# Performance work log

Measured on AMD Instinct MI355X. Metric: run time of the kernel, lower is better.

The kernel has to match this reference:

```python
import jax, jax.numpy as jnp
import numpy as np

B, S, D, H = 4, 8192, 1024, 16
DH = D // H  # attention head size


def setup_inputs() -> dict:
    key = jax.random.key(0)
    ks = jax.random.split(key, 12)
    sc = 0.02
    return {
        "hidden_states": jax.random.normal(ks[0], (B, S, D), jnp.float32),
        "attention_mask": jnp.zeros((B, 1, S), jnp.float32),
        "Wq": jax.random.normal(ks[1], (D, D), jnp.float32) * sc,
        "bq": jnp.zeros((D,), jnp.float32),
        "Wqa": jax.random.normal(ks[2], (D, H), jnp.float32) * sc,
        "bqa": jnp.zeros((H,), jnp.float32),
        "Wk": jax.random.normal(ks[3], (D, D), jnp.float32) * sc,
        "bk": jnp.zeros((D,), jnp.float32),
        "Wka": jax.random.normal(ks[4], (D, H), jnp.float32) * sc,
        "bka": jnp.zeros((H,), jnp.float32),
        "Wt": jax.random.normal(ks[5], (D, D), jnp.float32) * sc,
        "bt": jnp.zeros((D,), jnp.float32),
    }


def reference(hidden_states, attention_mask, Wq, bq, Wqa, bqa, Wk, bk, Wka, bka, Wt, bt):
    b, s, _ = hidden_states.shape
    scale = 1.0 / np.sqrt(DH).astype(np.float32)

    mixed_q = hidden_states @ Wq + bq            # [B,S,D]
    mixed_k = hidden_states @ Wk + bk            # [B,S,D]

    # query attention pooling: scores [B,H,S]
    q_score = (mixed_q @ Wqa + bqa).transpose(0, 2, 1) * scale + attention_mask
    q_weight = jax.nn.softmax(q_score, axis=-1)  # [B,H,S]

    q_heads = mixed_q.reshape(b, s, H, DH)       # [B,S,H,DH]
    pooled_q = jnp.einsum("bhs,bshd->bhd", q_weight, q_heads)  # [B,H,DH]
    pooled_q = pooled_q.reshape(b, 1, D)         # global query vector per batch

    mixed_qk = mixed_k * pooled_q                # [B,S,D]

    qk_score = (mixed_qk @ Wka + bka).transpose(0, 2, 1) * scale + attention_mask
    qk_weight = jax.nn.softmax(qk_score, axis=-1)  # [B,H,S]

    k_heads = mixed_qk.reshape(b, s, H, DH)
    pooled_k = jnp.einsum("bhs,bshd->bhd", qk_weight, k_heads)  # [B,H,DH]

    weighted = (q_heads * pooled_k[:, None, :, :]).reshape(b, s, D)  # [B,S,D]
    return weighted @ Wt + bt + mixed_q
```

## Files before the change

kernel.cpp:

```cpp
#include <hip/hip_runtime.h>
#include <hip/hip_bf16.h>
#include <stdint.h>

typedef __hip_bfloat16 bf16;
typedef __attribute__((ext_vector_type(8))) short bf16x8v;
typedef __attribute__((ext_vector_type(4))) float f32x4v;

#define B_   4
#define S_   8192
#define D_   1024
#define H_   16
#define DH_  64
#define M_TOT (B_ * S_)

__device__ __forceinline__ float bf2f(bf16 x) { return __bfloat162float(x); }
__device__ __forceinline__ bf16  f2bf(float x) { return __float2bfloat16(x); }

__device__ __forceinline__ void storev(float* p, float v) { *p = v; }
__device__ __forceinline__ void storev(bf16* p, float v) { *p = f2bf(v); }

__device__ __forceinline__ void async_copy16(const void* g, void* l) {
  __builtin_amdgcn_global_load_lds(
      (const __attribute__((address_space(1))) unsigned int*)g,
      (__attribute__((address_space(3))) unsigned int*)l,
      16, 0, 0);
}

#define VMCNT(n) asm volatile("s_waitcnt vmcnt(" #n ")" ::: "memory")
__device__ __forceinline__ void barrier_() {
  asm volatile("" ::: "memory");
  __builtin_amdgcn_s_barrier();
  asm volatile("" ::: "memory");
}

__global__ __launch_bounds__(256) void f2bf_kernel(
    const float* __restrict__ in, bf16* __restrict__ out, int n4)
{
  const int i = blockIdx.x * 256 + threadIdx.x;
  if (i >= n4) return;
  const float4 v = ((const float4*)in)[i];
  union { bf16 h[4]; uint64_t u; } pk;
  pk.h[0] = f2bf(v.x); pk.h[1] = f2bf(v.y);
  pk.h[2] = f2bf(v.z); pk.h[3] = f2bf(v.w);
  ((uint64_t*)out)[i] = pk.u;
}

#define STAGE_A(nb, h, k0) do { \
  async_copy16(gA + (size_t)((h) * 64      ) * sA + (size_t)(k0) * 2, smem + (nb) + (h) * 16384 + ldsw); \
  async_copy16(gA + (size_t)((h) * 64 + 128) * sA + (size_t)(k0) * 2, smem + (nb) + (h) * 16384 + 8192 + ldsw); \
} while (0)

#define STAGE_B(nb, h, k0) do { \
  async_copy16(gB + (size_t)((h) * 32      ) * sB + (size_t)(k0) * 2, smem + (nb) + 32768 + (h) * 16384 + ldsw); \
  async_copy16(gB + (size_t)((h) * 32 + 128) * sB + (size_t)(k0) * 2, smem + (nb) + 32768 + (h) * 16384 + 8192 + ldsw); \
} while (0)

#define READ_A(mh) do { \
  _Pragma("unroll") for (int il = 0; il < 4; ++il) { \
    const uint8_t* p_ = Ab + (mh) * 16384 + (wr * 64 + il * 16 + l16) * 128; \
    a[il][0] = *(const bf16x8v*)(p_ + k0off); \
    a[il][1] = *(const bf16x8v*)(p_ + k1off); } \
} while (0)

#define READ_B(nh, BR) do { \
  _Pragma("unroll") for (int jl = 0; jl < 2; ++jl) { \
    const uint8_t* p_ = Bb + 32768 + (nh) * 16384 + (wc * 32 + jl * 16 + l16) * 128; \
    BR[jl][0] = *(const bf16x8v*)(p_ + k0off); \
    BR[jl][1] = *(const bf16x8v*)(p_ + k1off); } \
} while (0)

#define MFMA_Q(IOFF, JOFF, BR) do { \
  _Pragma("unroll") for (int il = 0; il < 4; ++il) \
  _Pragma("unroll") for (int jl = 0; jl < 2; ++jl) \
  _Pragma("unroll") for (int kk = 0; kk < 2; ++kk) \
    acc[(IOFF) + il][(JOFF) + jl] = __builtin_amdgcn_mfma_f32_16x16x32_bf16( \
        a[il][kk], BR[jl][kk], acc[(IOFF) + il][(JOFF) + jl], 0, 0, 0); \
} while (0)

template <typename OutT>
__global__ __launch_bounds__(512, 2) void gemm256_kernel(
    const bf16* __restrict__ A, int lda, const bf16* __restrict__ BT,
    const float* __restrict__ bias0, const float* __restrict__ bias1,
    const bf16* addC, int ldadd,
    OutT* __restrict__ C, int ldc, int M, int Ncols, int K, int perBatchB)
{
  extern __shared__ __align__(16) uint8_t smem[];

  const int ntile = Ncols >> 8;
  const int mtiles = M >> 8;
  const int xcd = blockIdx.x & 7;
  const int local = blockIdx.x >> 3;
  const int tn = local % ntile;
  const int tm = xcd * (mtiles >> 3) + local / ntile;
  const int m0 = tm << 8, n0 = tn << 8;
  const bf16* Bt = BT + (perBatchB ? (size_t)(m0 >> 13) * (size_t)Ncols * (size_t)K : 0);

  const int tid = threadIdx.x, w = tid >> 6, lane = tid & 63;
  const int quad = lane >> 4, l16 = lane & 15;
  const int wr = w >> 2, wc = w & 3;
  const int lr = lane >> 3, ls = lane & 7;

  const size_t sA = (size_t)lda * 2, sB = (size_t)K * 2;
  const int srcslot = (ls ^ lr) << 4;
  const uint8_t* gA = (const uint8_t*)A  + (size_t)(m0 + 8 * w + lr) * sA + srcslot;
  const uint8_t* gB = (const uint8_t*)Bt + (size_t)(n0 + 64 * wr + 8 * wc + lr) * sB + srcslot;
  const int ldsw = w << 10;

  const int e7 = l16 & 7;
  const int k0off = (quad ^ e7) << 4;
  const int k1off = ((quad + 4) ^ e7) << 4;

  f32x4v acc[8][4] = {};
  bf16x8v a[4][2], b0[2][2], b1[2][2];

  const int NT = K >> 6;

  STAGE_A(0, 0, 0);
  STAGE_B(0, 0, 0);
  STAGE_B(0, 1, 0);
  STAGE_A(0, 1, 0);
  VMCNT(4);
  barrier_();

  for (int t = 0; t < NT; ++t) {
    const int buf = (t & 1) << 16;
    const int nbuf = buf ^ 65536;
    const int kst = (t + 1 < NT ? t + 1 : t) << 6;
    const uint8_t* Ab = smem + buf;
    const uint8_t* Bb = smem + buf;

    READ_A(0);
    READ_B(0, b0);
    STAGE_A(nbuf, 0, kst);
    barrier_();
    __builtin_amdgcn_s_setprio(1);
    MFMA_Q(0, 0, b0);
    __builtin_amdgcn_s_setprio(0);
    VMCNT(4);
    barrier_();

    READ_B(1, b1);
    STAGE_B(nbuf, 0, kst);
    barrier_();
    __builtin_amdgcn_s_setprio(1);
    MFMA_Q(0, 2, b1);
    __builtin_amdgcn_s_setprio(0);
    VMCNT(4);
    barrier_();

    READ_A(1);
    STAGE_B(nbuf, 1, kst);
    barrier_();
    __builtin_amdgcn_s_setprio(1);
    MFMA_Q(4, 2, b1);
    __builtin_amdgcn_s_setprio(0);
    barrier_();

    STAGE_A(nbuf, 1, kst);
    barrier_();
    __builtin_amdgcn_s_setprio(1);
    MFMA_Q(4, 0, b0);
    __builtin_amdgcn_s_setprio(0);
    VMCNT(4);
    barrier_();
  }
  VMCNT(0);

#pragma unroll
  for (int ai = 0; ai < 8; ++ai) {
    const int row = m0 + wr * 128 + ai * 16 + quad * 4;
#pragma unroll
    for (int jb = 0; jb < 4; ++jb) {
      const int col = n0 + wc * 64 + jb * 16 + l16;
      const float bb = (col < 1024) ? (bias0 ? bias0[col] : 0.f)
                                    : (bias1 ? bias1[col - 1024] : 0.f);
      f32x4v v = acc[ai][jb];
#pragma unroll
      for (int r = 0; r < 4; ++r) {
        float o = v[r] + bb;
        if (addC) o += bf2f(addC[(size_t)(row + r) * ldadd + col]);
        storev(&C[(size_t)(row + r) * ldc + col], o);
      }
    }
  }
}

__global__ __launch_bounds__(256) void score_kernel(
    const bf16* __restrict__ X, int ldx, const bf16* __restrict__ WaT,
    float* __restrict__ scores, int perBatchW)
{
  const int tid = threadIdx.x, wave = tid >> 6, lane = tid & 63;
  const int quad = lane >> 4, l16 = lane & 15;
  const int row0 = blockIdx.x * 64 + wave * 16;
  const int b = row0 / S_;
  const bf16* W = WaT + (perBatchW ? (size_t)b * H_ * D_ : 0);
  const bf16* arow = X + (size_t)(row0 + l16) * ldx;
  const bf16* brow = W + (size_t)l16 * D_;
  f32x4v acc = {};
  for (int k0 = 0; k0 < D_; k0 += 32) {
    bf16x8v av = *(const bf16x8v*)(arow + k0 + quad * 8);
    bf16x8v bv = *(const bf16x8v*)(brow + k0 + quad * 8);
    acc = __builtin_amdgcn_mfma_f32_16x16x32_bf16(av, bv, acc, 0, 0, 0);
  }
  const int srel = (row0 % S_) + quad * 4;
  float* orow = scores + ((size_t)b * H_ + l16) * S_ + srel;
#pragma unroll
  for (int r = 0; r < 4; r++) orow[r] = acc[r];
}

__global__ __launch_bounds__(256) void stats_kernel(
    const float* __restrict__ sc, const float* __restrict__ mask,
    float scale, float* __restrict__ stats)
{
  const int bh = blockIdx.x, b = bh >> 4, tid = threadIdx.x;
  const float* row = sc + (size_t)bh * S_;
  const float* mrow = mask + (size_t)b * S_;
  __shared__ float red[256];
  float m = -3.4e38f;
  for (int s = tid; s < S_; s += 256) m = fmaxf(m, row[s] * scale + mrow[s]);
  red[tid] = m; __syncthreads();
  for (int o = 128; o > 0; o >>= 1) { if (tid < o) red[tid] = fmaxf(red[tid], red[tid + o]); __syncthreads(); }
  const float M = red[0]; __syncthreads();
  float sum = 0.f;
  for (int s = tid; s < S_; s += 256) sum += expf(row[s] * scale + mrow[s] - M);
  red[tid] = sum; __syncthreads();
  for (int o = 128; o > 0; o >>= 1) { if (tid < o) red[tid] += red[tid + o]; __syncthreads(); }
  if (tid == 0) { stats[bh * 2] = M; stats[bh * 2 + 1] = red[0]; }
}

__global__ __launch_bounds__(256) void pool_kernel(
    const float* __restrict__ sc, const float* __restrict__ mask,
    const float* __restrict__ stats, const bf16* __restrict__ X, int ldx,
    float* __restrict__ pooled, float scale)
{
  const int bh = blockIdx.x, chunk = blockIdx.y;
  const int b = bh >> 4, h = bh & 15;
  const int dh = threadIdx.x & 63, sr = threadIdx.x >> 6;
  const float M = stats[bh * 2], inv = 1.f / stats[bh * 2 + 1];
  const float* row = sc + (size_t)bh * S_;
  const float* mrow = mask + (size_t)b * S_;
  float acc = 0.f;
  const int s0 = chunk * 256;
  for (int s = s0 + sr; s < s0 + 256; s += 4) {
    float w = expf(row[s] * scale + mrow[s] - M) * inv;
    acc += w * bf2f(X[((size_t)b * S_ + s) * ldx + h * DH_ + dh]);
  }
  __shared__ float red[256];
  red[threadIdx.x] = acc; __syncthreads();
  if (sr == 0)
    atomicAdd(&pooled[b * D_ + h * DH_ + dh],
              red[dh] + red[64 + dh] + red[128 + dh] + red[192 + dh]);
}

__global__ __launch_bounds__(256) void prep_wa_kernel(
    const float* __restrict__ Wa, const float* __restrict__ pq,
    bf16* __restrict__ out, int nb)
{
  const int idx = blockIdx.x * 256 + threadIdx.x;
  if (idx >= nb * H_ * D_) return;
  const int d = idx & (D_ - 1);
  const int h = (idx >> 10) & 15;
  const int b = idx >> 14;
  float v = Wa[d * H_ + h];
  if (pq) v *= pq[b * D_ + d];
  out[idx] = f2bf(v);
}

__global__ __launch_bounds__(1024) void transpose_kernel(
    const float* __restrict__ W, bf16* __restrict__ WT)
{
  __shared__ float t[32][33];
  const int tx = threadIdx.x, ty = threadIdx.y;
  const int bx = blockIdx.x, by = blockIdx.y;
  t[ty][tx] = W[(size_t)(by * 32 + ty) * D_ + bx * 32 + tx];
  __syncthreads();
  WT[(size_t)(bx * 32 + ty) * D_ + by * 32 + tx] = f2bf(t[tx][ty]);
}

__global__ __launch_bounds__(1024) void transpose_scale_kernel(
    const float* __restrict__ W, const float* __restrict__ pq,
    const float* __restrict__ pk, bf16* __restrict__ out)
{
  __shared__ float t[32][33];
  const int tx = threadIdx.x, ty = threadIdx.y;
  const int bx = blockIdx.x, by = blockIdx.y, b = blockIdx.z;
  t[ty][tx] = W[(size_t)(by * 32 + ty) * D_ + bx * 32 + tx];
  __syncthreads();
  const int n = bx * 32 + ty, k = by * 32 + tx;
  const float s = pq[b * D_ + k] * pk[b * D_ + k];
  out[(size_t)b * D_ * D_ + (size_t)n * D_ + k] = f2bf(t[tx][ty] * s);
}

namespace {
struct LdsAttrInit {
  LdsAttrInit() {
    (void)hipFuncSetAttribute(reinterpret_cast<const void*>(&gemm256_kernel<bf16>),
                              hipFuncAttributeMaxDynamicSharedMemorySize, 131072);
    (void)hipFuncSetAttribute(reinterpret_cast<const void*>(&gemm256_kernel<float>),
                              hipFuncAttributeMaxDynamicSharedMemorySize, 131072);
  }
};
LdsAttrInit ldsAttrInit_;
}

extern "C" void kernel_launch(void* const* d_in, const int* in_sizes, int n_in,
                              void* d_out, int out_size, void* d_ws, size_t ws_size,
                              hipStream_t stream)
{
  const float* hs   = (const float*)d_in[0];
  const float* mask = (const float*)d_in[1];
  const float* Wq   = (const float*)d_in[2];
  const float* bq   = (const float*)d_in[3];
  const float* Wqa  = (const float*)d_in[4];
  const float* Wk   = (const float*)d_in[6];
  const float* bk   = (const float*)d_in[7];
  const float* Wka  = (const float*)d_in[8];
  const float* Wt   = (const float*)d_in[10];
  const float* bt   = (const float*)d_in[11];
  float* out = (float*)d_out;

  uint8_t* w = (uint8_t*)d_ws;
  bf16*  hs_bf     = (bf16*)(w + 0);
  bf16*  mixed_qk  = (bf16*)(w + 67108864);
  bf16*  WqkT      = (bf16*)(w + 201326592);
  bf16*  WtTs      = (bf16*)(w + 205520896);
  bf16*  WaqT      = (bf16*)(w + 213909504);
  bf16*  WakTs     = (bf16*)(w + 213942272);
  float* scores_q  = (float*)(w + 214073344);
  float* scores_qk = (float*)(w + 216170496);
  float* stats_q   = (float*)(w + 218267648);
  float* stats_qk  = (float*)(w + 218268160);
  float* pq_raw    = (float*)(w + 218268672);
  float* pk_raw    = (float*)(w + 218285056);

  const bf16* mixed_q = mixed_qk;
  const bf16* mixed_k = mixed_qk + 1024;
  const int LDQK = 2048;

  const float scale = 0.125f;
  dim3 tblk(32, 32);

  f2bf_kernel<<<(M_TOT * D_ / 4 + 255) / 256, 256, 0, stream>>>(hs, hs_bf, M_TOT * D_ / 4);

  transpose_kernel<<<dim3(32, 32), tblk, 0, stream>>>(Wq, WqkT);
  transpose_kernel<<<dim3(32, 32), tblk, 0, stream>>>(Wk, WqkT + 1024 * 1024);

  gemm256_kernel<bf16><<<1024, 512, 131072, stream>>>(
      hs_bf, 1024, WqkT, bq, bk, nullptr, 0, mixed_qk, LDQK, M_TOT, 2048, D_, 0);

  hipMemsetAsync(pq_raw, 0, 2 * D_ * B_ * sizeof(float), stream);

  prep_wa_kernel<<<64, 256, 0, stream>>>(Wqa, nullptr, WaqT, 1);
  score_kernel<<<512, 256, 0, stream>>>(mixed_q, LDQK, WaqT, scores_q, 0);
  stats_kernel<<<64, 256, 0, stream>>>(scores_q, mask, scale, stats_q);
  pool_kernel<<<dim3(64, 32), 256, 0, stream>>>(scores_q, mask, stats_q, mixed_q, LDQK, pq_raw, scale);

  prep_wa_kernel<<<256, 256, 0, stream>>>(Wka, pq_raw, WakTs, 4);
  score_kernel<<<512, 256, 0, stream>>>(mixed_k, LDQK, WakTs, scores_qk, 1);
  stats_kernel<<<64, 256, 0, stream>>>(scores_qk, mask, scale, stats_qk);
  pool_kernel<<<dim3(64, 32), 256, 0, stream>>>(scores_qk, mask, stats_qk, mixed_k, LDQK, pk_raw, scale);

  transpose_scale_kernel<<<dim3(32, 32, 4), tblk, 0, stream>>>(Wt, pq_raw, pk_raw, WtTs);

  gemm256_kernel<float><<<512, 512, 131072, stream>>>(
      mixed_q, LDQK, WtTs, bt, nullptr, mixed_q, LDQK, out, D_, M_TOT, D_, D_, 1);
}
```

Baseline: 626.3 us.

## Unroll GEMM main loop by two, merge transposes, online softmax stats

```diff
diff --git a/kernel.cpp b/kernel.cpp
--- a/kernel.cpp
+++ b/kernel.cpp
@@ -27,6 +27,7 @@
 }
 
 #define VMCNT(n) asm volatile("s_waitcnt vmcnt(" #n ")" ::: "memory")
+#define LGKMCNT(n) asm volatile("s_waitcnt lgkmcnt(" #n ")" ::: "memory")
 __device__ __forceinline__ void barrier_() {
   asm volatile("" ::: "memory");
   __builtin_amdgcn_s_barrier();
@@ -36,13 +37,13 @@
 __global__ __launch_bounds__(256) void f2bf_kernel(
     const float* __restrict__ in, bf16* __restrict__ out, int n4)
 {
-  const int i = blockIdx.x * 256 + threadIdx.x;
-  if (i >= n4) return;
-  const float4 v = ((const float4*)in)[i];
-  union { bf16 h[4]; uint64_t u; } pk;
-  pk.h[0] = f2bf(v.x); pk.h[1] = f2bf(v.y);
-  pk.h[2] = f2bf(v.z); pk.h[3] = f2bf(v.w);
-  ((uint64_t*)out)[i] = pk.u;
+  for (int i = blockIdx.x * 256 + threadIdx.x; i < n4; i += 2048 * 256) {
+    const float4 v = ((const float4*)in)[i];
+    union { bf16 h[4]; uint64_t u; } pk;
+    pk.h[0] = f2bf(v.x); pk.h[1] = f2bf(v.y);
+    pk.h[2] = f2bf(v.z); pk.h[3] = f2bf(v.w);
+    ((uint64_t*)out)[i] = pk.u;
+  }
 }
 
 #define STAGE_A(nb, h, k0) do { \
@@ -75,6 +76,33 @@
   _Pragma("unroll") for (int kk = 0; kk < 2; ++kk) \
     acc[(IOFF) + il][(JOFF) + jl] = __builtin_amdgcn_mfma_f32_16x16x32_bf16( \
         a[il][kk], BR[jl][kk], acc[(IOFF) + il][(JOFF) + jl], 0, 0, 0); \
+} while (0)
+
+#define TILE(BUF, NBUF, KST, DOSTG, W0, W1, W3) do { \
+  const uint8_t* Ab = smem + (BUF); \
+  const uint8_t* Bb = smem + (BUF); \
+   \
+  READ_A(0); READ_B(0, b0); \
+  if (DOSTG) { STAGE_A((NBUF), 0, (KST)); STAGE_B((NBUF), 0, (KST)); } \
+  LGKMCNT(8); \
+  barrier_(); \
+  __builtin_amdgcn_s_setprio(1); MFMA_Q(0, 0, b0); __builtin_amdgcn_s_setprio(0); \
+  W0; barrier_(); \
+   \
+  READ_B(1, b1); \
+  if (DOSTG) { STAGE_B((NBUF), 1, (KST)); } \
+  barrier_(); \
+  __builtin_amdgcn_s_setprio(1); MFMA_Q(0, 2, b1); __builtin_amdgcn_s_setprio(0); \
+  W1; barrier_(); \
+   \
+  READ_A(1); \
+  if (DOSTG) { STAGE_A((NBUF), 1, (KST)); } \
+  barrier_(); \
+  __builtin_amdgcn_s_setprio(1); MFMA_Q(4, 2, b1); __builtin_amdgcn_s_setprio(0); \
+  barrier_(); \
+   \
+  __builtin_amdgcn_s_setprio(1); MFMA_Q(4, 0, b0); __builtin_amdgcn_s_setprio(0); \
+  W3; barrier_(); \
 } while (0)
 
 template <typename OutT>
@@ -122,49 +150,12 @@
   VMCNT(4);
   barrier_();
 
-  for (int t = 0; t < NT; ++t) {
-    const int buf = (t & 1) << 16;
-    const int nbuf = buf ^ 65536;
-    const int kst = (t + 1 < NT ? t + 1 : t) << 6;
-    const uint8_t* Ab = smem + buf;
-    const uint8_t* Bb = smem + buf;
-
-    READ_A(0);
-    READ_B(0, b0);
-    STAGE_A(nbuf, 0, kst);
-    barrier_();
-    __builtin_amdgcn_s_setprio(1);
-    MFMA_Q(0, 0, b0);
-    __builtin_amdgcn_s_setprio(0);
-    VMCNT(4);
-    barrier_();
-
-    READ_B(1, b1);
-    STAGE_B(nbuf, 0, kst);
-    barrier_();
-    __builtin_amdgcn_s_setprio(1);
-    MFMA_Q(0, 2, b1);
-    __builtin_amdgcn_s_setprio(0);
-    VMCNT(4);
-    barrier_();
-
-    READ_A(1);
-    STAGE_B(nbuf, 1, kst);
-    barrier_();
-    __builtin_amdgcn_s_setprio(1);
-    MFMA_Q(4, 2, b1);
-    __builtin_amdgcn_s_setprio(0);
-    barrier_();
-
-    STAGE_A(nbuf, 1, kst);
-    barrier_();
-    __builtin_amdgcn_s_setprio(1);
-    MFMA_Q(4, 0, b0);
-    __builtin_amdgcn_s_setprio(0);
-    VMCNT(4);
-    barrier_();
-  }
-  VMCNT(0);
+  for (int p = 0; p < (NT >> 1) - 1; ++p) {
+    TILE(0,     65536, (2 * p + 1) << 6, 1, VMCNT(6), VMCNT(6), VMCNT(4));
+    TILE(65536, 0,     (2 * p + 2) << 6, 1, VMCNT(6), VMCNT(6), VMCNT(4));
+  }
+  TILE(0,     65536, (NT - 1) << 6, 1, VMCNT(6), VMCNT(6), VMCNT(4));
+  TILE(65536, 0,     0,             0, VMCNT(2), VMCNT(0), (void)0);
 
 #pragma unroll
   for (int ai = 0; ai < 8; ++ai) {
@@ -213,19 +204,29 @@
     float scale, float* __restrict__ stats)
 {
   const int bh = blockIdx.x, b = bh >> 4, tid = threadIdx.x;
-  const float* row = sc + (size_t)bh * S_;
-  const float* mrow = mask + (size_t)b * S_;
-  __shared__ float red[256];
-  float m = -3.4e38f;
-  for (int s = tid; s < S_; s += 256) m = fmaxf(m, row[s] * scale + mrow[s]);
-  red[tid] = m; __syncthreads();
-  for (int o = 128; o > 0; o >>= 1) { if (tid < o) red[tid] = fmaxf(red[tid], red[tid + o]); __syncthreads(); }
-  const float M = red[0]; __syncthreads();
-  float sum = 0.f;
-  for (int s = tid; s < S_; s += 256) sum += expf(row[s] * scale + mrow[s] - M);
-  red[tid] = sum; __syncthreads();
-  for (int o = 128; o > 0; o >>= 1) { if (tid < o) red[tid] += red[tid + o]; __syncthreads(); }
-  if (tid == 0) { stats[bh * 2] = M; stats[bh * 2 + 1] = red[0]; }
+  const float4* row = (const float4*)(sc + (size_t)bh * S_);
+  const float4* mrow = (const float4*)(mask + (size_t)b * S_);
+  float m = -3.4e38f, l = 0.f;
+  for (int i = tid; i < S_ / 4; i += 256) {
+    const float4 r = row[i], k = mrow[i];
+    const float v0 = r.x * scale + k.x, v1 = r.y * scale + k.y;
+    const float v2 = r.z * scale + k.z, v3 = r.w * scale + k.w;
+    const float mx = fmaxf(fmaxf(v0, v1), fmaxf(v2, v3));
+    if (mx > m) { l *= expf(m - mx); m = mx; }
+    l += expf(v0 - m) + expf(v1 - m) + expf(v2 - m) + expf(v3 - m);
+  }
+  __shared__ float rm[256], rl[256];
+  rm[tid] = m; rl[tid] = l; __syncthreads();
+  for (int o = 128; o > 0; o >>= 1) {
+    if (tid < o) {
+      const float m2 = rm[tid + o], l2 = rl[tid + o];
+      const float M = fmaxf(rm[tid], m2);
+      rl[tid] = rl[tid] * expf(rm[tid] - M) + l2 * expf(m2 - M);
+      rm[tid] = M;
+    }
+    __syncthreads();
+  }
+  if (tid == 0) { stats[bh * 2] = rm[0]; stats[bh * 2 + 1] = rl[0]; }
 }
 
 __global__ __launch_bounds__(256) void pool_kernel(
@@ -266,15 +267,17 @@
   out[idx] = f2bf(v);
 }
 
-__global__ __launch_bounds__(1024) void transpose_kernel(
-    const float* __restrict__ W, bf16* __restrict__ WT)
+__global__ __launch_bounds__(1024) void transpose2_kernel(
+    const float* __restrict__ Wa, const float* __restrict__ Wb, bf16* __restrict__ WT)
 {
   __shared__ float t[32][33];
+  const float* W = blockIdx.z ? Wb : Wa;
+  bf16* out = WT + (size_t)blockIdx.z * 1024 * 1024;
   const int tx = threadIdx.x, ty = threadIdx.y;
   const int bx = blockIdx.x, by = blockIdx.y;
   t[ty][tx] = W[(size_t)(by * 32 + ty) * D_ + bx * 32 + tx];
   __syncthreads();
-  WT[(size_t)(bx * 32 + ty) * D_ + by * 32 + tx] = f2bf(t[tx][ty]);
+  out[(size_t)(bx * 32 + ty) * D_ + by * 32 + tx] = f2bf(t[tx][ty]);
 }
 
 __global__ __launch_bounds__(1024) void transpose_scale_kernel(
@@ -340,10 +343,9 @@
   const float scale = 0.125f;
   dim3 tblk(32, 32);
 
-  f2bf_kernel<<<(M_TOT * D_ / 4 + 255) / 256, 256, 0, stream>>>(hs, hs_bf, M_TOT * D_ / 4);
-
-  transpose_kernel<<<dim3(32, 32), tblk, 0, stream>>>(Wq, WqkT);
-  transpose_kernel<<<dim3(32, 32), tblk, 0, stream>>>(Wk, WqkT + 1024 * 1024);
+  f2bf_kernel<<<2048, 256, 0, stream>>>(hs, hs_bf, M_TOT * D_ / 4);
+
+  transpose2_kernel<<<dim3(32, 32, 2), tblk, 0, stream>>>(Wq, Wk, WqkT);
 
   gemm256_kernel<bf16><<<1024, 512, 131072, stream>>>(
       hs_bf, 1024, WqkT, bq, bk, nullptr, 0, mixed_qk, LDQK, M_TOT, 2048, D_, 0);
```

Result: no change. 628.4 us (+0.3%).
